# Optimization experiments

Hardware: AMD Instinct MI355X
Metric: run time of the kernel (lower is better)

## Reference

```python
import jax, jax.numpy as jnp
import numpy as np

N_P = 100000
N_A = 100000
IN = 128
H = 4
D = 32
E = 500000
ALPHA = 0.2


def _leaky(x, a=ALPHA):
    return jnp.where(x > 0, x, a * x)


def _gat_relation(Wh_src_rel, Wh_dst_self, a_src, a_dst, src, dst, n_dst):
    # Wh_src_rel: [Ns,H,D] relation-transformed source feats
    # Wh_dst_self: [Nd,H,D] self-transformed dest feats
    # a_src, a_dst: [H,D] attention vectors; src/dst: [E] edge index
    es = jnp.einsum('nhd,hd->nh', Wh_src_rel, a_src)  # [Ns,H]
    ed = jnp.einsum('nhd,hd->nh', Wh_dst_self, a_dst)  # [Nd,H]
    e = _leaky(es[src] + ed[dst])                      # [E,H]
    m = jax.ops.segment_max(e, dst, num_segments=n_dst)
    m = jnp.where(jnp.isfinite(m), m, 0.0)             # empty segments
    m = jax.lax.stop_gradient(m)
    ee = jnp.exp(e - m[dst])
    s = jax.ops.segment_sum(ee, dst, num_segments=n_dst)
    a = ee / s[dst]                                    # edge_softmax [E,H]
    msg = Wh_src_rel[src] * a[:, :, None]              # [E,H,D]
    return jax.ops.segment_sum(msg, dst, num_segments=n_dst)  # [Nd,H,D]


def setup_inputs() -> dict:
    key = jax.random.key(0)
    ks = jax.random.split(key, 32)
    inp = {
        'feat_P': jax.random.normal(ks[0], (N_P, IN), jnp.float32),
        'feat_A': jax.random.normal(ks[1], (N_A, IN), jnp.float32),
    }
    names = ['p2p', 'p2a', 'a2p', 'a2a']
    nsrc = {'p2p': N_P, 'p2a': N_P, 'a2p': N_A, 'a2a': N_A}
    ndst = {'p2p': N_P, 'p2a': N_A, 'a2p': N_P, 'a2a': N_A}
    for i, r in enumerate(names):
        inp['src_' + r] = jax.random.randint(ks[2 + 2 * i], (E,), 0, nsrc[r], jnp.int32)
        inp['dst_' + r] = jax.random.randint(ks[3 + 2 * i], (E,), 0, ndst[r], jnp.int32)
    # linear weights (torch Linear: y = x @ W.T + b); store as [IN, H*D]
    sc = 1.0 / np.sqrt(IN)
    for i, nm in enumerate(['P', 'A', 'p2p', 'p2a', 'a2p', 'a2a']):
        inp['W_' + nm] = jax.random.uniform(ks[10 + i], (IN, H * D), jnp.float32, -sc, sc)
        inp['b_' + nm] = jax.random.uniform(ks[16 + i], (H * D,), jnp.float32, -sc, sc)
    # attention vectors [H,D]
    for i, nm in enumerate(['p2p_src', 'p2p_dst', 'p2a_src', 'p2a_dst',
                            'a2p_src', 'a2p_dst', 'a2a_src', 'a2a_dst']):
        inp['att_' + nm] = jax.random.normal(ks[22 + i], (H, D), jnp.float32) * 0.1
    return inp


def reference(feat_P, feat_A,
              src_p2p, dst_p2p, src_p2a, dst_p2a,
              src_a2p, dst_a2p, src_a2a, dst_a2a,
              W_P, b_P, W_A, b_A, W_p2p, b_p2p, W_p2a, b_p2a,
              W_a2p, b_a2p, W_a2a, b_a2a,
              att_p2p_src, att_p2p_dst, att_p2a_src, att_p2a_dst,
              att_a2p_src, att_a2p_dst, att_a2a_src, att_a2a_dst):
    lin = lambda x, W, b: (x @ W + b).reshape(-1, H, D)
    Whp = lin(feat_P, W_P, b_P)      # [N_P,H,D]
    Wha = lin(feat_A, W_A, b_A)      # [N_A,H,D]
    Whp2p = lin(feat_P, W_p2p, b_p2p)
    Whp2a = lin(feat_P, W_p2a, b_p2a)
    Wha2p = lin(feat_A, W_a2p, b_a2p)
    Wha2a = lin(feat_A, W_a2a, b_a2a)
    ft_p2p = _gat_relation(Whp2p, Whp, att_p2p_src, att_p2p_dst, src_p2p, dst_p2p, N_P)
    ft_p2a = _gat_relation(Whp2a, Wha, att_p2a_src, att_p2a_dst, src_p2a, dst_p2a, N_A)
    ft_a2p = _gat_relation(Wha2p, Whp, att_a2p_src, att_a2p_dst, src_a2p, dst_a2p, N_P)
    ft_a2a = _gat_relation(Wha2a, Wha, att_a2a_src, att_a2a_dst, src_a2a, dst_a2a, N_A)
    h_P = jax.nn.relu(Whp + ft_p2p + ft_a2p)
    h_A = jax.nn.relu(Wha + ft_p2a + ft_a2a)
    return h_P, h_A
```

## Files before the change

kernel.cpp:

```cpp
#include <hip/hip_runtime.h>
#include <float.h>

#define ALPHA 0.2f
__device__ __forceinline__ float leakyf(float x) { return x > 0.0f ? x : ALPHA * x; }

__device__ __forceinline__ float bf2f(unsigned short u) {
    return __uint_as_float((unsigned)u << 16);
}
__device__ __forceinline__ unsigned short f2bf(float f) {
    unsigned u = __float_as_uint(f);
    return (unsigned short)((u + 0x7FFFu + ((u >> 16) & 1u)) >> 16);
}
__device__ __forceinline__ float bflo(unsigned u) { return __uint_as_float(u << 16); }
__device__ __forceinline__ float bfhi(unsigned u) { return __uint_as_float(u & 0xFFFF0000u); }

typedef short bf16x8 __attribute__((ext_vector_type(8)));
typedef float f32x4 __attribute__((ext_vector_type(4)));

struct Ptr4i { const int* p0; const int* p1; const int* p2; const int* p3; };
struct PrepM { const float* W; const float* b; const float* attA; const float* attB; };

__global__ __launch_bounds__(256) void prep_kernel(
    PrepM m0, PrepM m1, PrepM m2, PrepM m3, PrepM m4, PrepM m5,
    bf16x8* __restrict__ wfrag, float* __restrict__ cd)
{
    int mi = blockIdx.x;
    PrepM mm = (mi == 0) ? m0 : (mi == 1) ? m1 : (mi == 2) ? m2 :
               (mi == 3) ? m3 : (mi == 4) ? m4 : m5;
    int part = blockIdx.y;
    for (int ii = 0; ii < 3; ++ii) {
        int c = part * 576 + threadIdx.x + 256 * ii;
        if (c >= part * 576 + 576) continue;
        int t = c >> 8;
        int kstep = (c >> 6) & 3;
        int l = c & 63;
        int k0 = kstep * 32 + (l >> 4) * 8;
        bf16x8 out;
        if (t < 8) {
            int col = t * 16 + (l & 15);
            #pragma unroll
            for (int j = 0; j < 8; ++j)
                out[j] = (short)f2bf(mm.W[(size_t)(k0 + j) * 128 + col]);
        } else {
            int cl = l & 15;
            const float* att = nullptr; int h = 0;
            if (cl < 4 && mm.attA) { att = mm.attA; h = cl; }
            else if (cl >= 4 && cl < 8 && mm.attB) { att = mm.attB; h = cl - 4; }
            #pragma unroll
            for (int j = 0; j < 8; ++j) {
                float s = 0.f;
                if (att) {
                    const float* wrow = mm.W + (size_t)(k0 + j) * 128 + h * 32;
                    for (int d = 0; d < 32; ++d) s += wrow[d] * att[h * 32 + d];
                }
                out[j] = (short)f2bf(s);
            }
        }
        wfrag[(size_t)mi * 2304 + c] = out;
    }
    if (part == 0 && threadIdx.x < 8) {
        int cl = threadIdx.x;
        float s = 0.f;
        const float* att = nullptr; int h = 0;
        if (cl < 4 && mm.attA) { att = mm.attA; h = cl; }
        else if (cl >= 4 && mm.attB) { att = mm.attB; h = cl - 4; }
        if (att) for (int d = 0; d < 32; ++d) s += mm.b[h * 32 + d] * att[h * 32 + d];
        cd[mi * 8 + cl] = s;
    }
}

__device__ __forceinline__ void mfma_compute_store(
    const short* xs_s, const short* wl_s, int row0, int N,
    const float* __restrict__ b, float* __restrict__ o32, unsigned short* __restrict__ o16,
    float* __restrict__ dotA, float* __restrict__ dotB, const float* __restrict__ cd)
{
    int l = threadIdx.x & 63, w = threadIdx.x >> 6;
    int cl = l & 15, gq = l >> 4;
    f32x4 acc[9];
    #pragma unroll
    for (int t = 0; t < 9; ++t) acc[t] = (f32x4){0.f, 0.f, 0.f, 0.f};
    int arow = w * 16 + cl;
    #pragma unroll
    for (int ks = 0; ks < 4; ++ks) {
        int k8 = ks * 4 + gq;
        bf16x8 a = *(const bf16x8*)((const char*)xs_s + arow * 256 + ((k8 * 16) ^ ((arow & 7) << 4)));
        #pragma unroll
        for (int t = 0; t < 9; ++t) {
            bf16x8 bf = *(const bf16x8*)((const char*)wl_s + ((t * 4 + ks) * 64 + l) * 16);
            acc[t] = __builtin_amdgcn_mfma_f32_16x16x32_bf16(a, bf, acc[t], 0, 0, 0);
        }
    }
    int rbase = row0 + w * 16 + gq * 4;
    #pragma unroll
    for (int t = 0; t < 8; ++t) {
        int col = t * 16 + cl;
        float bias = b[col];
        #pragma unroll
        for (int j = 0; j < 4; ++j) {
            int row = rbase + j;
            if (row < N) {
                float v = acc[t][j] + bias;
                if (o32) o32[(size_t)row * 128 + col] = v;
                else     o16[(size_t)row * 128 + col] = f2bf(v);
            }
        }
    }
    if (cl < 8) {
        float cdv = cd[cl];
        float* dp = (cl < 4) ? dotA : dotB;
        int h = cl & 3;
        if (dp) {
            #pragma unroll
            for (int j = 0; j < 4; ++j) {
                int row = rbase + j;
                if (row < N) dp[(size_t)row * 4 + h] = acc[8][j] + cdv;
            }
        }
    }
}

__global__ __launch_bounds__(256) void lin3_mfma_kernel(
    const float* __restrict__ x, int N,
    const bf16x8* __restrict__ wfrag, const float* __restrict__ cd,
    const float* __restrict__ b0, float* __restrict__ o0, float* __restrict__ dA0, float* __restrict__ dB0,
    const float* __restrict__ b1, unsigned short* __restrict__ o1, float* __restrict__ dA1,
    const float* __restrict__ b2, unsigned short* __restrict__ o2, float* __restrict__ dA2)
{
    __shared__ short xs_s[64 * 128];
    __shared__ short wl_s[2304 * 8];
    const int row0 = blockIdx.x * 64;

    #pragma unroll
    for (int ii = 0; ii < 4; ++ii) {
        int c = threadIdx.x + 256 * ii;
        int r = c >> 4, k8 = c & 15;
        int srcrow = row0 + r; if (srcrow >= N) srcrow = N - 1;
        const float4* gp = (const float4*)(x + (size_t)srcrow * 128 + k8 * 8);
        float4 v0 = gp[0], v1 = gp[1];
        bf16x8 p;
        p[0] = (short)f2bf(v0.x); p[1] = (short)f2bf(v0.y);
        p[2] = (short)f2bf(v0.z); p[3] = (short)f2bf(v0.w);
        p[4] = (short)f2bf(v1.x); p[5] = (short)f2bf(v1.y);
        p[6] = (short)f2bf(v1.z); p[7] = (short)f2bf(v1.w);
        *(bf16x8*)((char*)xs_s + r * 256 + ((k8 * 16) ^ ((r & 7) << 4))) = p;
    }
    #pragma unroll
    for (int ii = 0; ii < 9; ++ii)
        ((bf16x8*)wl_s)[threadIdx.x + 256 * ii] = wfrag[threadIdx.x + 256 * ii];
    __syncthreads();
    mfma_compute_store(xs_s, wl_s, row0, N, b0, o0, nullptr, dA0, dB0, cd);

    __syncthreads();
    #pragma unroll
    for (int ii = 0; ii < 9; ++ii)
        ((bf16x8*)wl_s)[threadIdx.x + 256 * ii] = wfrag[2304 + threadIdx.x + 256 * ii];
    __syncthreads();
    mfma_compute_store(xs_s, wl_s, row0, N, b1, nullptr, o1, dA1, nullptr, cd + 8);

    __syncthreads();
    #pragma unroll
    for (int ii = 0; ii < 9; ++ii)
        ((bf16x8*)wl_s)[threadIdx.x + 256 * ii] = wfrag[2 * 2304 + threadIdx.x + 256 * ii];
    __syncthreads();
    mfma_compute_store(xs_s, wl_s, row0, N, b2, nullptr, o2, dA2, nullptr, cd + 16);
}

__global__ __launch_bounds__(256) void zero_kernel(int* __restrict__ p, int n) {
    int i = blockIdx.x * 256 + threadIdx.x;
    if (i < n) p[i] = 0;
}


__global__ __launch_bounds__(256) void binA_count_kernel(Ptr4i dsts, int* __restrict__ bcnt,
                                                         int nbkMax, int E)
{
    __shared__ int lh[128];
    if (threadIdx.x < 128) lh[threadIdx.x] = 0;
    __syncthreads();
    int r = blockIdx.y;
    const int* dst = (r == 0) ? dsts.p0 : (r == 1) ? dsts.p1 : (r == 2) ? dsts.p2 : dsts.p3;
    int base = blockIdx.x * 4096;
    #pragma unroll 4
    for (int ii = 0; ii < 16; ++ii) {
        int i = base + threadIdx.x + 256 * ii;
        if (i < E) atomicAdd(&lh[dst[i] >> 10], 1);
    }
    __syncthreads();
    if (threadIdx.x < nbkMax) {
        int v = lh[threadIdx.x];
        if (v) atomicAdd(&bcnt[r * nbkMax + threadIdx.x], v);
    }
}

__global__ __launch_bounds__(64) void bin_scan_kernel(const int* __restrict__ bcnt,
                                                      int* __restrict__ bbase,
                                                      int* __restrict__ gwptr, int nbkMax)
{
    int r = threadIdx.x;
    if (r >= 4) return;
    int run = 0;
    for (int b = 0; b < nbkMax; ++b) {
        int v = bcnt[r * nbkMax + b];
        bbase[r * nbkMax + b] = run;
        gwptr[r * nbkMax + b] = run;
        run += v;
    }
}

__global__ __launch_bounds__(256) void binA_scatter_kernel(Ptr4i dsts, Ptr4i srcs,
    int* __restrict__ gwptr, unsigned* __restrict__ packed, int nbkMax, int E)
{
    __shared__ int lh[128], loff[128], lptr[128], gb[128];
    __shared__ unsigned stg[4096];
    __shared__ unsigned short sb[4096];
    if (threadIdx.x < 128) lh[threadIdx.x] = 0;
    __syncthreads();
    int r = blockIdx.y;
    const int* dst = (r == 0) ? dsts.p0 : (r == 1) ? dsts.p1 : (r == 2) ? dsts.p2 : dsts.p3;
    const int* src = (r == 0) ? srcs.p0 : (r == 1) ? srcs.p1 : (r == 2) ? srcs.p2 : srcs.p3;
    int base = blockIdx.x * 4096;
    int d16[16], s16[16];
    #pragma unroll 4
    for (int ii = 0; ii < 16; ++ii) {
        int i = base + threadIdx.x + 256 * ii;
        if (i < E) {
            d16[ii] = dst[i];
            s16[ii] = src[i];
            atomicAdd(&lh[d16[ii] >> 10], 1);
        } else d16[ii] = -1;
    }
    __syncthreads();
    if (threadIdx.x == 0) {
        int run = 0;
        for (int b = 0; b < nbkMax; ++b) { loff[b] = run; lptr[b] = run; run += lh[b]; }
    }
    __syncthreads();
    #pragma unroll 4
    for (int ii = 0; ii < 16; ++ii) {
        if (d16[ii] >= 0) {
            int b = d16[ii] >> 10;
            int p = atomicAdd(&lptr[b], 1);
            stg[p] = ((unsigned)s16[ii] << 10) | (unsigned)(d16[ii] & 1023);
            sb[p] = (unsigned short)b;
        }
    }
    __syncthreads();
    if (threadIdx.x < nbkMax && lh[threadIdx.x])
        gb[threadIdx.x] = atomicAdd(&gwptr[r * nbkMax + threadIdx.x], lh[threadIdx.x]);
    __syncthreads();
    int tot = min(4096, E - base);
    #pragma unroll 4
    for (int ii = 0; ii < 16; ++ii) {
        int p = threadIdx.x + 256 * ii;
        if (p < tot) {
            int b = sb[p];
            packed[(size_t)r * E + gb[b] + (p - loff[b])] = stg[p];
        }
    }
}

__global__ __launch_bounds__(256) void binB_build_kernel(
    const unsigned* __restrict__ packed, const int* __restrict__ bcnt, const int* __restrict__ bbase,
    int nbkMax, int4 Ns, int E, int stride,
    int* __restrict__ start, int* __restrict__ deg, int* __restrict__ csrc)
{
    int r = blockIdx.y, b = blockIdx.x;
    int N = (r == 0) ? Ns.x : (r == 1) ? Ns.y : (r == 2) ? Ns.z : Ns.w;
    int dst0 = b << 10;
    if (dst0 >= N) return;
    int cnt  = bcnt[r * nbkMax + b];
    int base = bbase[r * nbkMax + b];
    __shared__ int hist[1024];
    __shared__ int sums[256];
    #pragma unroll
    for (int i = 0; i < 4; ++i) hist[threadIdx.x * 4 + i] = 0;
    __syncthreads();
    const unsigned* pk = packed + (size_t)r * E + base;
    for (int i = threadIdx.x; i < cnt; i += 256)
        atomicAdd(&hist[pk[i] & 1023], 1);
    __syncthreads();
    int v4[4], s = 0;
    #pragma unroll
    for (int i = 0; i < 4; ++i) { v4[i] = hist[threadIdx.x * 4 + i]; s += v4[i]; }
    sums[threadIdx.x] = s;
    __syncthreads();
    #pragma unroll
    for (int off = 1; off < 256; off <<= 1) {
        int y = (threadIdx.x >= off) ? sums[threadIdx.x - off] : 0;
        __syncthreads();
        sums[threadIdx.x] += y;
        __syncthreads();
    }
    int run = sums[threadIdx.x] - s;
    int* st = start + (size_t)r * stride;
    int* dg = deg   + (size_t)r * stride;
    #pragma unroll
    for (int i = 0; i < 4; ++i) {
        int idx = threadIdx.x * 4 + i;
        int d = dst0 + idx;
        if (d < N) { dg[d] = v4[i]; st[d] = base + run; }
        hist[idx] = run;
        run += v4[i];
    }
    __syncthreads();
    int* cs = csrc + (size_t)r * E + base;
    for (int i = threadIdx.x; i < cnt; i += 256) {
        unsigned e = pk[i];
        int p = atomicAdd(&hist[e & 1023], 1);
        cs[p] = (int)(e >> 10);
    }
}

__global__ __launch_bounds__(256) void gat_node_kernel(
    float* __restrict__ out, int Nd,
    const int* __restrict__ start0, const int* __restrict__ deg0, const int* __restrict__ csrc0,
    const unsigned short* __restrict__ Wh0, const float* __restrict__ es0, const float* __restrict__ ed0,
    const int* __restrict__ start1, const int* __restrict__ deg1, const int* __restrict__ csrc1,
    const unsigned short* __restrict__ Wh1, const float* __restrict__ es1, const float* __restrict__ ed1)
{
    int gid = blockIdx.x * 256 + threadIdx.x;
    int d = gid >> 6;
    if (d >= Nd) return;
    int lane = threadIdx.x & 63;
    int q = lane >> 4;
    int l = lane & 15;
    int h = l >> 2;

    const float4* orow = (const float4*)(out + (size_t)d * 128);
    float4 A0 = orow[l * 2], A1 = orow[l * 2 + 1];

    #pragma unroll
    for (int rel = 0; rel < 2; ++rel) {
        const int* start = rel ? start1 : start0;
        const int* deg   = rel ? deg1   : deg0;
        const int* csrc  = rel ? csrc1  : csrc0;
        const unsigned short* Wh = rel ? Wh1 : Wh0;
        const float* es  = rel ? es1 : es0;
        const float* ed  = rel ? ed1 : ed0;

        int st = start[d];
        int n  = deg[d];
        if (n == 0) continue;
        float edv = ed[(size_t)d * 4 + h];
        float sum = 0.f;
        float m0 = 0.f, m1 = 0.f, m2 = 0.f, m3 = 0.f;
        float m4 = 0.f, m5 = 0.f, m6 = 0.f, m7 = 0.f;
        for (int j = q; j < n; j += 4) {
            int s = csrc[st + j];
            float p = __expf(leakyf(es[(size_t)s * 4 + h] + edv));
            uint4 w = ((const uint4*)(Wh + (size_t)s * 128))[l];
            sum += p;
            m0 += p * bflo(w.x); m1 += p * bfhi(w.x);
            m2 += p * bflo(w.y); m3 += p * bfhi(w.y);
            m4 += p * bflo(w.z); m5 += p * bfhi(w.z);
            m6 += p * bflo(w.w); m7 += p * bfhi(w.w);
        }
        #pragma unroll
        for (int off = 16; off < 64; off <<= 1) {
            sum += __shfl_xor(sum, off, 64);
            m0 += __shfl_xor(m0, off, 64); m1 += __shfl_xor(m1, off, 64);
            m2 += __shfl_xor(m2, off, 64); m3 += __shfl_xor(m3, off, 64);
            m4 += __shfl_xor(m4, off, 64); m5 += __shfl_xor(m5, off, 64);
            m6 += __shfl_xor(m6, off, 64); m7 += __shfl_xor(m7, off, 64);
        }
        float inv = 1.0f / sum;
        A0.x += m0 * inv; A0.y += m1 * inv; A0.z += m2 * inv; A0.w += m3 * inv;
        A1.x += m4 * inv; A1.y += m5 * inv; A1.z += m6 * inv; A1.w += m7 * inv;
    }
    if (lane < 16) {
        A0.x = fmaxf(A0.x, 0.f); A0.y = fmaxf(A0.y, 0.f);
        A0.z = fmaxf(A0.z, 0.f); A0.w = fmaxf(A0.w, 0.f);
        A1.x = fmaxf(A1.x, 0.f); A1.y = fmaxf(A1.y, 0.f);
        A1.z = fmaxf(A1.z, 0.f); A1.w = fmaxf(A1.w, 0.f);
        float4* ow = (float4*)(out + (size_t)d * 128);
        ow[l * 2] = A0; ow[l * 2 + 1] = A1;
    }
}

extern "C" void kernel_launch(void* const* d_in, const int* in_sizes, int n_in,
                              void* d_out, int out_size, void* d_ws, size_t ws_size,
                              hipStream_t stream)
{
    const float* feat_P = (const float*)d_in[0];
    const float* feat_A = (const float*)d_in[1];
    const int* src_p2p = (const int*)d_in[2];
    const int* dst_p2p = (const int*)d_in[3];
    const int* src_p2a = (const int*)d_in[4];
    const int* dst_p2a = (const int*)d_in[5];
    const int* src_a2p = (const int*)d_in[6];
    const int* dst_a2p = (const int*)d_in[7];
    const int* src_a2a = (const int*)d_in[8];
    const int* dst_a2a = (const int*)d_in[9];
    const float* W_P   = (const float*)d_in[10]; const float* b_P   = (const float*)d_in[11];
    const float* W_A   = (const float*)d_in[12]; const float* b_A   = (const float*)d_in[13];
    const float* W_p2p = (const float*)d_in[14]; const float* b_p2p = (const float*)d_in[15];
    const float* W_p2a = (const float*)d_in[16]; const float* b_p2a = (const float*)d_in[17];
    const float* W_a2p = (const float*)d_in[18]; const float* b_a2p = (const float*)d_in[19];
    const float* W_a2a = (const float*)d_in[20]; const float* b_a2a = (const float*)d_in[21];
    const float* att_p2p_src = (const float*)d_in[22];
    const float* att_p2p_dst = (const float*)d_in[23];
    const float* att_p2a_src = (const float*)d_in[24];
    const float* att_p2a_dst = (const float*)d_in[25];
    const float* att_a2p_src = (const float*)d_in[26];
    const float* att_a2p_dst = (const float*)d_in[27];
    const float* att_a2a_src = (const float*)d_in[28];
    const float* att_a2a_dst = (const float*)d_in[29];

    const int NP = in_sizes[0] / 128;
    const int NA = in_sizes[1] / 128;
    const int E  = in_sizes[2];
    const int stride = (NP > NA) ? NP : NA;
    const int nbkMax = (stride + 1023) >> 10;

    float* outP = (float*)d_out;
    float* outA = (float*)d_out + (size_t)NP * 128;

    char* ws = (char*)d_ws;
    size_t off = 0;
    auto alloc = [&](size_t bytes) -> void* {
        void* p = ws + off;
        off += (bytes + 255) & ~(size_t)255;
        return p;
    };
    unsigned short* Whp2p = (unsigned short*)alloc((size_t)NP * 128 * 2);
    unsigned short* Whp2a = (unsigned short*)alloc((size_t)NP * 128 * 2);
    unsigned short* Wha2p = (unsigned short*)alloc((size_t)NA * 128 * 2);
    unsigned short* Wha2a = (unsigned short*)alloc((size_t)NA * 128 * 2);
    float* es_p2p = (float*)alloc((size_t)NP * 16);
    float* es_p2a = (float*)alloc((size_t)NP * 16);
    float* es_a2p = (float*)alloc((size_t)NA * 16);
    float* es_a2a = (float*)alloc((size_t)NA * 16);
    float* ed_p2p = (float*)alloc((size_t)NP * 16);
    float* ed_a2p = (float*)alloc((size_t)NP * 16);
    float* ed_p2a = (float*)alloc((size_t)NA * 16);
    float* ed_a2a = (float*)alloc((size_t)NA * 16);
    int* deg    = (int*)alloc((size_t)4 * stride * 4);
    int* start  = (int*)alloc((size_t)4 * stride * 4);
    int* csrc   = (int*)alloc((size_t)4 * E * 4);
    unsigned* packed = (unsigned*)alloc((size_t)4 * E * 4);
    int* bcnt   = (int*)alloc((size_t)4 * nbkMax * 4);
    int* bbase  = (int*)alloc((size_t)4 * nbkMax * 4);
    int* gwptr  = (int*)alloc((size_t)4 * nbkMax * 4);
    bf16x8* wfrag = (bf16x8*)alloc((size_t)6 * 2304 * 16);
    float* cd     = (float*)alloc((size_t)6 * 8 * 4);

    Ptr4i dsts = {dst_p2p, dst_a2p, dst_p2a, dst_a2a};
    Ptr4i srcs = {src_p2p, src_a2p, src_p2a, src_a2a};
    int4 Ns = make_int4(NP, NP, NA, NA);

    {
        PrepM m0 = {W_P,   b_P,   att_p2p_dst, att_a2p_dst};
        PrepM m1 = {W_p2p, b_p2p, att_p2p_src, nullptr};
        PrepM m2 = {W_p2a, b_p2a, att_p2a_src, nullptr};
        PrepM m3 = {W_A,   b_A,   att_p2a_dst, att_a2a_dst};
        PrepM m4 = {W_a2p, b_a2p, att_a2p_src, nullptr};
        PrepM m5 = {W_a2a, b_a2a, att_a2a_src, nullptr};
        prep_kernel<<<dim3(6, 4), 256, 0, stream>>>(m0, m1, m2, m3, m4, m5, wfrag, cd);
    }

    lin3_mfma_kernel<<<(NP + 63) / 64, 256, 0, stream>>>(feat_P, NP,
        wfrag, cd,
        b_P,   outP,  ed_p2p, ed_a2p,
        b_p2p, Whp2p, es_p2p,
        b_p2a, Whp2a, es_p2a);
    lin3_mfma_kernel<<<(NA + 63) / 64, 256, 0, stream>>>(feat_A, NA,
        wfrag + (size_t)3 * 2304, cd + 24,
        b_A,   outA,  ed_p2a, ed_a2a,
        b_a2p, Wha2p, es_a2p,
        b_a2a, Wha2a, es_a2a);

    zero_kernel<<<(4 * nbkMax + 255) / 256, 256, 0, stream>>>(bcnt, 4 * nbkMax);
    {
        dim3 gA((E + 4095) / 4096, 4);
        binA_count_kernel<<<gA, 256, 0, stream>>>(dsts, bcnt, nbkMax, E);
        bin_scan_kernel<<<1, 64, 0, stream>>>(bcnt, bbase, gwptr, nbkMax);
        binA_scatter_kernel<<<gA, 256, 0, stream>>>(dsts, srcs, gwptr, packed, nbkMax, E);
        binB_build_kernel<<<dim3(nbkMax, 4), 256, 0, stream>>>(packed, bcnt, bbase,
            nbkMax, Ns, E, stride, start, deg, csrc);
    }

    gat_node_kernel<<<(NP * 64 + 255) / 256, 256, 0, stream>>>(outP, NP,
        start + 0 * (size_t)stride, deg + 0 * (size_t)stride, csrc + 0 * (size_t)E, Whp2p, es_p2p, ed_p2p,
        start + 1 * (size_t)stride, deg + 1 * (size_t)stride, csrc + 1 * (size_t)E, Wha2p, es_a2p, ed_a2p);
    gat_node_kernel<<<(NA * 64 + 255) / 256, 256, 0, stream>>>(outA, NA,
        start + 2 * (size_t)stride, deg + 2 * (size_t)stride, csrc + 2 * (size_t)E, Whp2a, es_p2a, ed_p2a,
        start + 3 * (size_t)stride, deg + 3 * (size_t)stride, csrc + 3 * (size_t)E, Wha2a, es_a2a, ed_a2a);
}
```

Measured before the change: 374.6 us.

## Merge P/A launches, fold zeroing into prep, parallelize bin scan, unroll gather

Merges the paired P and A launches of the linear MFMA kernel and the GAT node kernel into single grids that pick their config by block index. The bin-count zeroing moves into the prep kernel, so one launch disappears. The bin scan becomes a parallel Hillis-Steele scan over 512 threads instead of a serial loop on 4 threads. The count kernel uses per-wave shared histograms, and the GAT edge loop is unrolled by two to put more gathers in flight. Together these are meant to cut launch overhead and tail gaps, at the cost of more register pressure from the unroll.

Measured after the change: 336.7 us. -10.1%, faster.

```diff
diff --git a/kernel.cpp b/kernel.cpp
--- a/kernel.cpp
+++ b/kernel.cpp
@@ -4,9 +4,6 @@
 #define ALPHA 0.2f
 __device__ __forceinline__ float leakyf(float x) { return x > 0.0f ? x : ALPHA * x; }
 
-__device__ __forceinline__ float bf2f(unsigned short u) {
-    return __uint_as_float((unsigned)u << 16);
-}
 __device__ __forceinline__ unsigned short f2bf(float f) {
     unsigned u = __float_as_uint(f);
     return (unsigned short)((u + 0x7FFFu + ((u >> 16) & 1u)) >> 16);
@@ -22,12 +19,16 @@
 
 __global__ __launch_bounds__(256) void prep_kernel(
     PrepM m0, PrepM m1, PrepM m2, PrepM m3, PrepM m4, PrepM m5,
-    bf16x8* __restrict__ wfrag, float* __restrict__ cd)
+    bf16x8* __restrict__ wfrag, float* __restrict__ cd,
+    int* __restrict__ bcnt, int nz)
 {
     int mi = blockIdx.x;
     PrepM mm = (mi == 0) ? m0 : (mi == 1) ? m1 : (mi == 2) ? m2 :
                (mi == 3) ? m3 : (mi == 4) ? m4 : m5;
     int part = blockIdx.y;
+    if (mi == 0 && part == 0) {
+        for (int i = threadIdx.x; i < nz; i += 256) bcnt[i] = 0;
+    }
     for (int ii = 0; ii < 3; ++ii) {
         int c = part * 576 + threadIdx.x + 256 * ii;
         if (c >= part * 576 + 576) continue;
@@ -119,23 +120,30 @@
     }
 }
 
-__global__ __launch_bounds__(256) void lin3_mfma_kernel(
-    const float* __restrict__ x, int N,
-    const bf16x8* __restrict__ wfrag, const float* __restrict__ cd,
-    const float* __restrict__ b0, float* __restrict__ o0, float* __restrict__ dA0, float* __restrict__ dB0,
-    const float* __restrict__ b1, unsigned short* __restrict__ o1, float* __restrict__ dA1,
-    const float* __restrict__ b2, unsigned short* __restrict__ o2, float* __restrict__ dA2)
+struct Lin3Cfg {
+    const float* x; int N; int blocks;
+    const bf16x8* wfrag; const float* cd;
+    const float* b0; float* o0; float* dA0; float* dB0;
+    const float* b1; unsigned short* o1; float* dA1;
+    const float* b2; unsigned short* o2; float* dA2;
+};
+
+__global__ __launch_bounds__(256) void lin3_mfma_kernel(Lin3Cfg cP, Lin3Cfg cA)
 {
     __shared__ short xs_s[64 * 128];
     __shared__ short wl_s[2304 * 8];
-    const int row0 = blockIdx.x * 64;
+    const bool isP = blockIdx.x < (unsigned)cP.blocks;
+    const Lin3Cfg& c = isP ? cP : cA;
+    const int bx = isP ? blockIdx.x : (blockIdx.x - cP.blocks);
+    const int row0 = bx * 64;
+    const int N = c.N;
 
     #pragma unroll
     for (int ii = 0; ii < 4; ++ii) {
-        int c = threadIdx.x + 256 * ii;
-        int r = c >> 4, k8 = c & 15;
+        int ci = threadIdx.x + 256 * ii;
+        int r = ci >> 4, k8 = ci & 15;
         int srcrow = row0 + r; if (srcrow >= N) srcrow = N - 1;
-        const float4* gp = (const float4*)(x + (size_t)srcrow * 128 + k8 * 8);
+        const float4* gp = (const float4*)(c.x + (size_t)srcrow * 128 + k8 * 8);
         float4 v0 = gp[0], v1 = gp[1];
         bf16x8 p;
         p[0] = (short)f2bf(v0.x); p[1] = (short)f2bf(v0.y);
@@ -146,64 +154,69 @@
     }
     #pragma unroll
     for (int ii = 0; ii < 9; ++ii)
-        ((bf16x8*)wl_s)[threadIdx.x + 256 * ii] = wfrag[threadIdx.x + 256 * ii];
-    __syncthreads();
-    mfma_compute_store(xs_s, wl_s, row0, N, b0, o0, nullptr, dA0, dB0, cd);
+        ((bf16x8*)wl_s)[threadIdx.x + 256 * ii] = c.wfrag[threadIdx.x + 256 * ii];
+    __syncthreads();
+    mfma_compute_store(xs_s, wl_s, row0, N, c.b0, c.o0, nullptr, c.dA0, c.dB0, c.cd);
 
     __syncthreads();
     #pragma unroll
     for (int ii = 0; ii < 9; ++ii)
-        ((bf16x8*)wl_s)[threadIdx.x + 256 * ii] = wfrag[2304 + threadIdx.x + 256 * ii];
-    __syncthreads();
-    mfma_compute_store(xs_s, wl_s, row0, N, b1, nullptr, o1, dA1, nullptr, cd + 8);
+        ((bf16x8*)wl_s)[threadIdx.x + 256 * ii] = c.wfrag[2304 + threadIdx.x + 256 * ii];
+    __syncthreads();
+    mfma_compute_store(xs_s, wl_s, row0, N, c.b1, nullptr, c.o1, c.dA1, nullptr, c.cd + 8);
 
     __syncthreads();
     #pragma unroll
     for (int ii = 0; ii < 9; ++ii)
-        ((bf16x8*)wl_s)[threadIdx.x + 256 * ii] = wfrag[2 * 2304 + threadIdx.x + 256 * ii];
-    __syncthreads();
-    mfma_compute_store(xs_s, wl_s, row0, N, b2, nullptr, o2, dA2, nullptr, cd + 16);
-}
-
-__global__ __launch_bounds__(256) void zero_kernel(int* __restrict__ p, int n) {
-    int i = blockIdx.x * 256 + threadIdx.x;
-    if (i < n) p[i] = 0;
+        ((bf16x8*)wl_s)[threadIdx.x + 256 * ii] = c.wfrag[2 * 2304 + threadIdx.x + 256 * ii];
+    __syncthreads();
+    mfma_compute_store(xs_s, wl_s, row0, N, c.b2, nullptr, c.o2, c.dA2, nullptr, c.cd + 16);
 }
 
 
 __global__ __launch_bounds__(256) void binA_count_kernel(Ptr4i dsts, int* __restrict__ bcnt,
                                                          int nbkMax, int E)
 {
-    __shared__ int lh[128];
-    if (threadIdx.x < 128) lh[threadIdx.x] = 0;
+    __shared__ int lh[4][128];
+    ((int*)lh)[threadIdx.x] = 0;
+    ((int*)lh)[threadIdx.x + 256] = 0;
     __syncthreads();
     int r = blockIdx.y;
+    int w = threadIdx.x >> 6;
     const int* dst = (r == 0) ? dsts.p0 : (r == 1) ? dsts.p1 : (r == 2) ? dsts.p2 : dsts.p3;
     int base = blockIdx.x * 4096;
     #pragma unroll 4
     for (int ii = 0; ii < 16; ++ii) {
         int i = base + threadIdx.x + 256 * ii;
-        if (i < E) atomicAdd(&lh[dst[i] >> 10], 1);
-    }
-    __syncthreads();
-    if (threadIdx.x < nbkMax) {
-        int v = lh[threadIdx.x];
-        if (v) atomicAdd(&bcnt[r * nbkMax + threadIdx.x], v);
-    }
-}
-
-__global__ __launch_bounds__(64) void bin_scan_kernel(const int* __restrict__ bcnt,
-                                                      int* __restrict__ bbase,
-                                                      int* __restrict__ gwptr, int nbkMax)
-{
-    int r = threadIdx.x;
-    if (r >= 4) return;
-    int run = 0;
-    for (int b = 0; b < nbkMax; ++b) {
-        int v = bcnt[r * nbkMax + b];
-        bbase[r * nbkMax + b] = run;
-        gwptr[r * nbkMax + b] = run;
-        run += v;
+        if (i < E) atomicAdd(&lh[w][dst[i] >> 10], 1);
+    }
+    __syncthreads();
+    if (threadIdx.x < 128) {
+        int v = lh[0][threadIdx.x] + lh[1][threadIdx.x] + lh[2][threadIdx.x] + lh[3][threadIdx.x];
+        if (v && threadIdx.x < nbkMax) atomicAdd(&bcnt[r * nbkMax + threadIdx.x], v);
+    }
+}
+
+__global__ __launch_bounds__(512) void bin_scan_kernel(const int* __restrict__ bcnt,
+                                                       int* __restrict__ bbase,
+                                                       int* __restrict__ gwptr, int nbkMax)
+{
+    __shared__ int sh[4][128];
+    int r = threadIdx.x >> 7, b = threadIdx.x & 127;
+    int v = (b < nbkMax) ? bcnt[r * nbkMax + b] : 0;
+    sh[r][b] = v;
+    __syncthreads();
+    #pragma unroll
+    for (int off = 1; off < 128; off <<= 1) {
+        int y = (b >= off) ? sh[r][b - off] : 0;
+        __syncthreads();
+        sh[r][b] += y;
+        __syncthreads();
+    }
+    if (b < nbkMax) {
+        int ex = sh[r][b] - v;
+        bbase[r * nbkMax + b] = ex;
+        gwptr[r * nbkMax + b] = ex;
     }
 }
 
@@ -311,49 +324,66 @@
     }
 }
 
-__global__ __launch_bounds__(256) void gat_node_kernel(
-    float* __restrict__ out, int Nd,
-    const int* __restrict__ start0, const int* __restrict__ deg0, const int* __restrict__ csrc0,
-    const unsigned short* __restrict__ Wh0, const float* __restrict__ es0, const float* __restrict__ ed0,
-    const int* __restrict__ start1, const int* __restrict__ deg1, const int* __restrict__ csrc1,
-    const unsigned short* __restrict__ Wh1, const float* __restrict__ es1, const float* __restrict__ ed1)
-{
-    int gid = blockIdx.x * 256 + threadIdx.x;
+struct GatRel {
+    const int* start; const int* deg; const int* csrc;
+    const unsigned short* Wh; const float* es; const float* ed;
+};
+struct GatCfg { float* out; int Nd; int blocks; GatRel rel0, rel1; };
+
+__global__ __launch_bounds__(256) void gat_node_kernel(GatCfg cP, GatCfg cA)
+{
+    const bool isP = blockIdx.x < (unsigned)cP.blocks;
+    const GatCfg& c = isP ? cP : cA;
+    const int bx = isP ? blockIdx.x : (blockIdx.x - cP.blocks);
+    int gid = bx * 256 + threadIdx.x;
     int d = gid >> 6;
-    if (d >= Nd) return;
+    if (d >= c.Nd) return;
     int lane = threadIdx.x & 63;
     int q = lane >> 4;
     int l = lane & 15;
     int h = l >> 2;
 
-    const float4* orow = (const float4*)(out + (size_t)d * 128);
+    const float4* orow = (const float4*)(c.out + (size_t)d * 128);
     float4 A0 = orow[l * 2], A1 = orow[l * 2 + 1];
 
     #pragma unroll
     for (int rel = 0; rel < 2; ++rel) {
-        const int* start = rel ? start1 : start0;
-        const int* deg   = rel ? deg1   : deg0;
-        const int* csrc  = rel ? csrc1  : csrc0;
-        const unsigned short* Wh = rel ? Wh1 : Wh0;
-        const float* es  = rel ? es1 : es0;
-        const float* ed  = rel ? ed1 : ed0;
-
-        int st = start[d];
-        int n  = deg[d];
+        const GatRel& R = rel ? c.rel1 : c.rel0;
+        int st = R.start[d];
+        int n  = R.deg[d];
         if (n == 0) continue;
-        float edv = ed[(size_t)d * 4 + h];
+        const uint4* W4 = (const uint4*)R.Wh;
+        float edv = R.ed[(size_t)d * 4 + h];
         float sum = 0.f;
         float m0 = 0.f, m1 = 0.f, m2 = 0.f, m3 = 0.f;
         float m4 = 0.f, m5 = 0.f, m6 = 0.f, m7 = 0.f;
-        for (int j = q; j < n; j += 4) {
-            int s = csrc[st + j];
-            float p = __expf(leakyf(es[(size_t)s * 4 + h] + edv));
-            uint4 w = ((const uint4*)(Wh + (size_t)s * 128))[l];
-            sum += p;
-            m0 += p * bflo(w.x); m1 += p * bfhi(w.x);
-            m2 += p * bflo(w.y); m3 += p * bfhi(w.y);
-            m4 += p * bflo(w.z); m5 += p * bfhi(w.z);
-            m6 += p * bflo(w.w); m7 += p * bfhi(w.w);
+        int j = q;
+        for (; j + 4 < n; j += 8) {
+            int s0 = R.csrc[st + j];
+            int s1 = R.csrc[st + j + 4];
+            float p0 = __expf(leakyf(R.es[(size_t)s0 * 4 + h] + edv));
+            float p1 = __expf(leakyf(R.es[(size_t)s1 * 4 + h] + edv));
+            uint4 w0 = W4[(size_t)s0 * 16 + l];
+            uint4 w1 = W4[(size_t)s1 * 16 + l];
+            sum += p0 + p1;
+            m0 += p0 * bflo(w0.x) + p1 * bflo(w1.x);
+            m1 += p0 * bfhi(w0.x) + p1 * bfhi(w1.x);
+            m2 += p0 * bflo(w0.y) + p1 * bflo(w1.y);
+            m3 += p0 * bfhi(w0.y) + p1 * bfhi(w1.y);
+            m4 += p0 * bflo(w0.z) + p1 * bflo(w1.z);
+            m5 += p0 * bfhi(w0.z) + p1 * bfhi(w1.z);
+            m6 += p0 * bflo(w0.w) + p1 * bflo(w1.w);
+            m7 += p0 * bfhi(w0.w) + p1 * bfhi(w1.w);
+        }
+        if (j < n) {
+            int s0 = R.csrc[st + j];
+            float p0 = __expf(leakyf(R.es[(size_t)s0 * 4 + h] + edv));
+            uint4 w0 = W4[(size_t)s0 * 16 + l];
+            sum += p0;
+            m0 += p0 * bflo(w0.x); m1 += p0 * bfhi(w0.x);
+            m2 += p0 * bflo(w0.y); m3 += p0 * bfhi(w0.y);
+            m4 += p0 * bflo(w0.z); m5 += p0 * bfhi(w0.z);
+            m6 += p0 * bflo(w0.w); m7 += p0 * bfhi(w0.w);
         }
         #pragma unroll
         for (int off = 16; off < 64; off <<= 1) {
@@ -372,7 +402,7 @@
         A0.z = fmaxf(A0.z, 0.f); A0.w = fmaxf(A0.w, 0.f);
         A1.x = fmaxf(A1.x, 0.f); A1.y = fmaxf(A1.y, 0.f);
         A1.z = fmaxf(A1.z, 0.f); A1.w = fmaxf(A1.w, 0.f);
-        float4* ow = (float4*)(out + (size_t)d * 128);
+        float4* ow = (float4*)(c.out + (size_t)d * 128);
         ow[l * 2] = A0; ow[l * 2 + 1] = A1;
     }
 }
@@ -455,34 +485,38 @@
         PrepM m3 = {W_A,   b_A,   att_p2a_dst, att_a2a_dst};
         PrepM m4 = {W_a2p, b_a2p, att_a2p_src, nullptr};
         PrepM m5 = {W_a2a, b_a2a, att_a2a_src, nullptr};
-        prep_kernel<<<dim3(6, 4), 256, 0, stream>>>(m0, m1, m2, m3, m4, m5, wfrag, cd);
-    }
-
-    lin3_mfma_kernel<<<(NP + 63) / 64, 256, 0, stream>>>(feat_P, NP,
-        wfrag, cd,
-        b_P,   outP,  ed_p2p, ed_a2p,
-        b_p2p, Whp2p, es_p2p,
-        b_p2a, Whp2a, es_p2a);
-    lin3_mfma_kernel<<<(NA + 63) / 64, 256, 0, stream>>>(feat_A, NA,
-        wfrag + (size_t)3 * 2304, cd + 24,
-        b_A,   outA,  ed_p2a, ed_a2a,
-        b_a2p, Wha2p, es_a2p,
-        b_a2a, Wha2a, es_a2a);
-
-    zero_kernel<<<(4 * nbkMax + 255) / 256, 256, 0, stream>>>(bcnt, 4 * nbkMax);
+        prep_kernel<<<dim3(6, 4), 256, 0, stream>>>(m0, m1, m2, m3, m4, m5, wfrag, cd,
+                                                    bcnt, 4 * nbkMax);
+    }
+
+    {
+        Lin3Cfg cP = {feat_P, NP, (NP + 63) / 64, wfrag, cd,
+                      b_P, outP, ed_p2p, ed_a2p,
+                      b_p2p, Whp2p, es_p2p,
+                      b_p2a, Whp2a, es_p2a};
+        Lin3Cfg cA = {feat_A, NA, (NA + 63) / 64, wfrag + (size_t)3 * 2304, cd + 24,
+                      b_A, outA, ed_p2a, ed_a2a,
+                      b_a2p, Wha2p, es_a2p,
+                      b_a2a, Wha2a, es_a2a};
+        lin3_mfma_kernel<<<cP.blocks + cA.blocks, 256, 0, stream>>>(cP, cA);
+    }
+
     {
         dim3 gA((E + 4095) / 4096, 4);
         binA_count_kernel<<<gA, 256, 0, stream>>>(dsts, bcnt, nbkMax, E);
-        bin_scan_kernel<<<1, 64, 0, stream>>>(bcnt, bbase, gwptr, nbkMax);
+        bin_scan_kernel<<<1, 512, 0, stream>>>(bcnt, bbase, gwptr, nbkMax);
         binA_scatter_kernel<<<gA, 256, 0, stream>>>(dsts, srcs, gwptr, packed, nbkMax, E);
         binB_build_kernel<<<dim3(nbkMax, 4), 256, 0, stream>>>(packed, bcnt, bbase,
             nbkMax, Ns, E, stride, start, deg, csrc);
     }
 
-    gat_node_kernel<<<(NP * 64 + 255) / 256, 256, 0, stream>>>(outP, NP,
-        start + 0 * (size_t)stride, deg + 0 * (size_t)stride, csrc + 0 * (size_t)E, Whp2p, es_p2p, ed_p2p,
-        start + 1 * (size_t)stride, deg + 1 * (size_t)stride, csrc + 1 * (size_t)E, Wha2p, es_a2p, ed_a2p);
-    gat_node_kernel<<<(NA * 64 + 255) / 256, 256, 0, stream>>>(outA, NA,
-        start + 2 * (size_t)stride, deg + 2 * (size_t)stride, csrc + 2 * (size_t)E, Whp2a, es_p2a, ed_p2a,
-        start + 3 * (size_t)stride, deg + 3 * (size_t)stride, csrc + 3 * (size_t)E, Wha2a, es_a2a, ed_a2a);
-}
+    {
+        GatCfg cP = {outP, NP, (NP * 64 + 255) / 256,
+            {start + 0 * (size_t)stride, deg + 0 * (size_t)stride, csrc + 0 * (size_t)E, Whp2p, es_p2p, ed_p2p},
+            {start + 1 * (size_t)stride, deg + 1 * (size_t)stride, csrc + 1 * (size_t)E, Wha2p, es_a2p, ed_a2p}};
+        GatCfg cA = {outA, NA, (NA * 64 + 255) / 256,
+            {start + 2 * (size_t)stride, deg + 2 * (size_t)stride, csrc + 2 * (size_t)E, Whp2a, es_p2a, ed_p2a},
+            {start + 3 * (size_t)stride, deg + 3 * (size_t)stride, csrc + 3 * (size_t)E, Wha2a, es_a2a, ed_a2a}};
+        gat_node_kernel<<<cP.blocks + cA.blocks, 256, 0, stream>>>(cP, cA);
+    }
+}
```
